# Kernel tuning notes

Hardware: AMD Instinct MI355X
Metric: run time of the kernel (lower is better)

Reference implementation:

```python
import jax, jax.numpy as jnp
import numpy as np

N_NODES = 50000
N_EDGES = 800000
IN_CH, HID_CH, OUT_CH = 512, 128, 64


def gcn_conv(x, W, b, src, dst, num_nodes):
    """PyG GCNConv: add self-loops, sym-normalize, linear, scatter-add, bias.
    x: [N, Fin], W: [Fout, Fin], b: [Fout], src/dst: [E] int."""
    loop = jnp.arange(num_nodes, dtype=src.dtype)
    src2 = jnp.concatenate([src, loop])  # [E+N]
    dst2 = jnp.concatenate([dst, loop])
    deg = jax.ops.segment_sum(jnp.ones_like(dst2, dtype=x.dtype), dst2,
                              num_segments=num_nodes)  # in-degree + 1
    d_inv_sqrt = jnp.where(deg > 0, jax.lax.rsqrt(deg), 0.0)
    norm = d_inv_sqrt[src2] * d_inv_sqrt[dst2]  # [E+N]
    h = x @ W.T  # [N, Fout]
    msg = h[src2] * norm[:, None]  # [E+N, Fout] -- dominant memory traffic
    out = jax.ops.segment_sum(msg, dst2, num_segments=num_nodes)
    return out + b


def setup_inputs() -> dict:
    key = jax.random.key(0)
    ks = jax.random.split(key, 8)
    x = jax.random.normal(ks[0], (N_NODES, IN_CH), dtype=jnp.float32)
    edge_index = jax.random.randint(ks[1], (2, N_EDGES), 0, N_NODES, dtype=jnp.int64)
    s1 = 1.0 / np.sqrt(IN_CH)
    s2 = 1.0 / np.sqrt(HID_CH)
    W1 = jax.random.normal(ks[2], (HID_CH, IN_CH), dtype=jnp.float32) * s1
    b1 = jnp.zeros((HID_CH,), dtype=jnp.float32)
    W_mu = jax.random.normal(ks[3], (OUT_CH, HID_CH), dtype=jnp.float32) * s2
    b_mu = jnp.zeros((OUT_CH,), dtype=jnp.float32)
    W_logstd = jax.random.normal(ks[4], (OUT_CH, HID_CH), dtype=jnp.float32) * s2
    b_logstd = jnp.zeros((OUT_CH,), dtype=jnp.float32)
    return {"x": x, "edge_index": edge_index, "W1": W1, "b1": b1,
            "W_mu": W_mu, "b_mu": b_mu, "W_logstd": W_logstd, "b_logstd": b_logstd}


def reference(x, edge_index, W1, b1, W_mu, b_mu, W_logstd, b_logstd):
    src, dst = edge_index[0], edge_index[1]
    n = x.shape[0]
    h = jax.nn.relu(gcn_conv(x, W1, b1, src, dst, n))
    mu = gcn_conv(h, W_mu, b_mu, src, dst, n)
    logstd = gcn_conv(h, W_logstd, b_logstd, src, dst, n)
    return (mu, logstd)
```

## Files before the change

kernel.cpp:

```cpp
#include <hip/hip_runtime.h>

constexpr int FIN = 512;
constexpr int FH  = 128;
constexpr int FO  = 64;

typedef short short8 __attribute__((ext_vector_type(8)));
typedef float f32x4 __attribute__((ext_vector_type(4)));

__device__ __forceinline__ unsigned short f2bf(float f) {
    unsigned u = __float_as_uint(f);
    u += 0x7fffu + ((u >> 16) & 1u);
    return (unsigned short)(u >> 16);
}
__device__ __forceinline__ float bf2f(unsigned short h) {
    return __uint_as_float((unsigned)h << 16);
}
__device__ __forceinline__ float bflo(unsigned v) { return __uint_as_float(v << 16); }
__device__ __forceinline__ float bfhi(unsigned v) { return __uint_as_float(v & 0xffff0000u); }


__global__ void clear_kernel(int4* __restrict__ p, int n4) {
    int i = blockIdx.x * blockDim.x + threadIdx.x;
    if (i < n4) p[i] = make_int4(0, 0, 0, 0);
}


__global__ void pre_kernel(const int* __restrict__ dst, int* __restrict__ cnt, int E,
                           const float* __restrict__ W1, unsigned short* __restrict__ W1b,
                           const float* __restrict__ Wmu, const float* __restrict__ Wlg,
                           unsigned short* __restrict__ Wh, unsigned short* __restrict__ Wl,
                           int cntB) {
    int b = blockIdx.x;
    if (b < cntB) {
        int i = b * 256 + threadIdx.x;
        if (i < E) atomicAdd(&cnt[dst[i]], 1);
    } else if (b < cntB + 64) {
        int i = (b - cntB) * 256 + threadIdx.x;
        float4 v = ((const float4*)W1)[i];
        ushort4 p;
        p.x = f2bf(v.x); p.y = f2bf(v.y); p.z = f2bf(v.z); p.w = f2bf(v.w);
        ((ushort4*)W1b)[i] = p;
    } else {
        int i = (b - cntB - 64) * 256 + threadIdx.x;
        int r = i >> 7, c = i & 127;
        float f = (r < 64) ? Wmu[r * 128 + c] : Wlg[(r - 64) * 128 + c];
        unsigned short h = f2bf(f);
        Wh[i] = h;
        Wl[i] = f2bf(f - bf2f(h));
    }
}


__global__ void scan1_kernel(const int* __restrict__ cnt, int* __restrict__ offs,
                             int* __restrict__ bsum, float* __restrict__ dinv, int n) {
    __shared__ int sdata[256];
    int t = threadIdx.x;
    int base = blockIdx.x * 1024 + t * 4;
    int4 c = make_int4(0, 0, 0, 0);
    if (base + 3 < n) {
        c = *(const int4*)(cnt + base);
    } else {
        if (base + 0 < n) c.x = cnt[base + 0];
        if (base + 1 < n) c.y = cnt[base + 1];
        if (base + 2 < n) c.z = cnt[base + 2];
        if (base + 3 < n) c.w = cnt[base + 3];
    }
    if (base + 0 < n) dinv[base + 0] = rsqrtf((float)(c.x + 1));
    if (base + 1 < n) dinv[base + 1] = rsqrtf((float)(c.y + 1));
    if (base + 2 < n) dinv[base + 2] = rsqrtf((float)(c.z + 1));
    if (base + 3 < n) dinv[base + 3] = rsqrtf((float)(c.w + 1));

    int s0 = c.x + c.y + c.z + c.w;
    sdata[t] = s0;
    __syncthreads();
    for (int off = 1; off < 256; off <<= 1) {
        int v = (t >= off) ? sdata[t - off] : 0;
        __syncthreads();
        sdata[t] += v;
        __syncthreads();
    }
    int excl = sdata[t] - s0;
    if (t == 255) bsum[blockIdx.x] = sdata[255];
    if (base + 0 < n) offs[base + 0] = excl;
    if (base + 1 < n) offs[base + 1] = excl + c.x;
    if (base + 2 < n) offs[base + 2] = excl + c.x + c.y;
    if (base + 3 < n) offs[base + 3] = excl + c.x + c.y + c.z;
}

__global__ void scan2_kernel(int* __restrict__ bsum, int nb) {
    __shared__ int sdata[256];
    int t = threadIdx.x;
    int v = (t < nb) ? bsum[t] : 0;
    sdata[t] = v;
    __syncthreads();
    for (int off = 1; off < 256; off <<= 1) {
        int u = (t >= off) ? sdata[t - off] : 0;
        __syncthreads();
        sdata[t] += u;
        __syncthreads();
    }
    if (t < nb) bsum[t] = sdata[t] - v;
}

__global__ void scan3_kernel(int* __restrict__ offs, const int* __restrict__ bsum,
                             int n, int E) {
    int i = blockIdx.x * blockDim.x + threadIdx.x;
    if (i < n) offs[i] += bsum[i >> 10];
    if (i == 0) offs[n] = E;
}


__global__ void fill_kernel(const int* __restrict__ src, const int* __restrict__ dst,
                            const float* __restrict__ dinv, const int* __restrict__ offs,
                            int* __restrict__ cnt, int2* __restrict__ esort, int E) {
    int i = blockIdx.x * blockDim.x + threadIdx.x;
    if (i < E) {
        int s = src[i];
        int d = dst[i];
        int old = atomicSub(&cnt[d], 1);
        int pos = offs[d] + old - 1;
        float w = dinv[s] * dinv[d];
        esort[pos] = make_int2(s, __float_as_int(w));
    }
}


__global__ void spmm_kernel(const unsigned int* __restrict__ hin, const int* __restrict__ offs,
                            const int2* __restrict__ esort, const float* __restrict__ dinv,
                            const float* __restrict__ bias, unsigned int* __restrict__ hout,
                            int n, int relu) {
    int gid = blockIdx.x * blockDim.x + threadIdx.x;
    int node = gid >> 6;
    int lane = threadIdx.x & 63;
    if (node >= n) return;
    float di = dinv[node];
    unsigned hv = hin[(size_t)node * 64 + lane];
    float ax = di * di * bflo(hv);
    float ay = di * di * bfhi(hv);
    int p = offs[node];
    int end = offs[node + 1];
    if ((p & 1) && p < end) {
        int2 e = esort[p];
        unsigned v = hin[(size_t)e.x * 64 + lane];
        float w = __int_as_float(e.y);
        ax = fmaf(w, bflo(v), ax); ay = fmaf(w, bfhi(v), ay);
        ++p;
    }
    for (; p + 8 <= end; p += 8) {
        int4 q0 = *(const int4*)(esort + p + 0);
        int4 q1 = *(const int4*)(esort + p + 2);
        int4 q2 = *(const int4*)(esort + p + 4);
        int4 q3 = *(const int4*)(esort + p + 6);
        unsigned v0 = hin[(size_t)q0.x * 64 + lane];
        unsigned v1 = hin[(size_t)q0.z * 64 + lane];
        unsigned v2 = hin[(size_t)q1.x * 64 + lane];
        unsigned v3 = hin[(size_t)q1.z * 64 + lane];
        unsigned v4 = hin[(size_t)q2.x * 64 + lane];
        unsigned v5 = hin[(size_t)q2.z * 64 + lane];
        unsigned v6 = hin[(size_t)q3.x * 64 + lane];
        unsigned v7 = hin[(size_t)q3.z * 64 + lane];
        float w0 = __int_as_float(q0.y), w1 = __int_as_float(q0.w);
        float w2 = __int_as_float(q1.y), w3 = __int_as_float(q1.w);
        float w4 = __int_as_float(q2.y), w5 = __int_as_float(q2.w);
        float w6 = __int_as_float(q3.y), w7 = __int_as_float(q3.w);
        ax = fmaf(w0, bflo(v0), ax); ay = fmaf(w0, bfhi(v0), ay);
        ax = fmaf(w1, bflo(v1), ax); ay = fmaf(w1, bfhi(v1), ay);
        ax = fmaf(w2, bflo(v2), ax); ay = fmaf(w2, bfhi(v2), ay);
        ax = fmaf(w3, bflo(v3), ax); ay = fmaf(w3, bfhi(v3), ay);
        ax = fmaf(w4, bflo(v4), ax); ay = fmaf(w4, bfhi(v4), ay);
        ax = fmaf(w5, bflo(v5), ax); ay = fmaf(w5, bfhi(v5), ay);
        ax = fmaf(w6, bflo(v6), ax); ay = fmaf(w6, bfhi(v6), ay);
        ax = fmaf(w7, bflo(v7), ax); ay = fmaf(w7, bfhi(v7), ay);
    }
    for (; p + 2 <= end; p += 2) {
        int4 q = *(const int4*)(esort + p);
        unsigned v0 = hin[(size_t)q.x * 64 + lane];
        unsigned v1 = hin[(size_t)q.z * 64 + lane];
        float w0 = __int_as_float(q.y), w1 = __int_as_float(q.w);
        ax = fmaf(w0, bflo(v0), ax); ay = fmaf(w0, bfhi(v0), ay);
        ax = fmaf(w1, bflo(v1), ax); ay = fmaf(w1, bfhi(v1), ay);
    }
    if (p < end) {
        int2 e = esort[p];
        unsigned v = hin[(size_t)e.x * 64 + lane];
        float w = __int_as_float(e.y);
        ax = fmaf(w, bflo(v), ax); ay = fmaf(w, bfhi(v), ay);
    }
    if (bias) {
        float2 b = ((const float2*)bias)[lane];
        ax += b.x; ay += b.y;
    }
    if (relu) { ax = fmaxf(ax, 0.f); ay = fmaxf(ay, 0.f); }
    unsigned o = (unsigned)f2bf(ax) | ((unsigned)f2bf(ay) << 16);
    hout[(size_t)node * 64 + lane] = o;
}


__global__ __launch_bounds__(1024, 4) void gemm1_kernel(
    const float* __restrict__ X, const unsigned short* __restrict__ Wb,
    unsigned short* __restrict__ out, int M, int nstrips) {
    extern __shared__ __align__(16) unsigned short Bs[];
    int tid = threadIdx.x;

    #pragma unroll
    for (int j = 0; j < 8; ++j) {
        int f = tid + j * 1024;
        int row = f >> 6;
        unsigned addr = ((unsigned)f << 4) ^ ((unsigned)(row & 7) << 4);
        *(short8*)((char*)Bs + addr) = ((const short8*)Wb)[f];
    }
    __syncthreads();

    int lane = tid & 63, wid = tid >> 6;
    int fr = lane & 15, fq = lane >> 4;
    int s = wid * gridDim.x + blockIdx.x;
    if (s >= nstrips) return;
    int row0 = s * 16;
    int arow = row0 + fr; if (arow >= M) arow = M - 1;
    const float* ap = X + (size_t)arow * FIN + fq * 8;

    f32x4 acc[8] = {};

    float4 c0 = *(const float4*)(ap + 0);
    float4 c1 = *(const float4*)(ap + 4);
    float4 c2 = *(const float4*)(ap + 32);
    float4 c3 = *(const float4*)(ap + 36);

    #pragma unroll
    for (int kk = 0; kk < 8; ++kk) {
        int k0 = kk * 64;
        float4 d0 = c0, d1 = c1, d2 = c2, d3 = c3;
        if (kk < 7) {
            c0 = *(const float4*)(ap + k0 + 64);
            c1 = *(const float4*)(ap + k0 + 68);
            c2 = *(const float4*)(ap + k0 + 96);
            c3 = *(const float4*)(ap + k0 + 100);
        }
        short8 af0, af1;
        af0[0] = (short)f2bf(d0.x); af0[1] = (short)f2bf(d0.y);
        af0[2] = (short)f2bf(d0.z); af0[3] = (short)f2bf(d0.w);
        af0[4] = (short)f2bf(d1.x); af0[5] = (short)f2bf(d1.y);
        af0[6] = (short)f2bf(d1.z); af0[7] = (short)f2bf(d1.w);
        af1[0] = (short)f2bf(d2.x); af1[1] = (short)f2bf(d2.y);
        af1[2] = (short)f2bf(d2.z); af1[3] = (short)f2bf(d2.w);
        af1[4] = (short)f2bf(d3.x); af1[5] = (short)f2bf(d3.y);
        af1[6] = (short)f2bf(d3.z); af1[7] = (short)f2bf(d3.w);

        int cb0 = k0 * 2 + fq * 16;
        #pragma unroll
        for (int c = 0; c < 8; ++c) {
            int br = c * 16 + fr;
            short8 b0 = *(const short8*)((const char*)Bs + br * 1024 +
                                         ((unsigned)cb0 ^ ((unsigned)(br & 7) << 4)));
            acc[c] = __builtin_amdgcn_mfma_f32_16x16x32_bf16(af0, b0, acc[c], 0, 0, 0);
        }
        int cb1 = cb0 + 64;
        #pragma unroll
        for (int c = 0; c < 8; ++c) {
            int br = c * 16 + fr;
            short8 b1 = *(const short8*)((const char*)Bs + br * 1024 +
                                         ((unsigned)cb1 ^ ((unsigned)(br & 7) << 4)));
            acc[c] = __builtin_amdgcn_mfma_f32_16x16x32_bf16(af1, b1, acc[c], 0, 0, 0);
        }
    }

    #pragma unroll
    for (int c = 0; c < 8; ++c) {
        #pragma unroll
        for (int j = 0; j < 4; ++j) {
            int row = row0 + fq * 4 + j;
            if (row < M) out[(size_t)row * FH + c * 16 + fr] = f2bf(acc[c][j]);
        }
    }
}


__global__ __launch_bounds__(512) void gemm2_kernel(
    const unsigned short* __restrict__ Xb,
    const unsigned short* __restrict__ Wh, const unsigned short* __restrict__ Wl,
    float* __restrict__ outA, float* __restrict__ outB,
    const float* __restrict__ biasA, const float* __restrict__ biasB,
    int M, int nstrips) {
    __shared__ __align__(16) unsigned short WhS[128 * 128];
    __shared__ __align__(16) unsigned short WlS[128 * 128];
    int tid = threadIdx.x;

    #pragma unroll
    for (int j = 0; j < 4; ++j) {
        int f = tid + j * 512;
        int row = f >> 4;
        unsigned addr = ((unsigned)f * 16u) ^ ((unsigned)(row & 7) << 4);
        *(short8*)((char*)WhS + addr) = ((const short8*)Wh)[f];
        *(short8*)((char*)WlS + addr) = ((const short8*)Wl)[f];
    }
    __syncthreads();

    int lane = tid & 63, wid = tid >> 6;
    int fr = lane & 15, fq = lane >> 4;
    int s = blockIdx.x * 8 + wid;
    if (s >= nstrips) return;
    int row0 = s * 16;
    int arow = row0 + fr; if (arow > M - 1) arow = M - 1;
    const unsigned short* ap = Xb + (size_t)arow * FH + fq * 8;

    short8 a0 = *(const short8*)(ap + 0);
    short8 a1 = *(const short8*)(ap + 32);
    short8 a2 = *(const short8*)(ap + 64);
    short8 a3 = *(const short8*)(ap + 96);

    f32x4 acc[8] = {};

    auto proc = [&](int k0, short8 a) {
        int cb = k0 * 2 + fq * 16;
        #pragma unroll
        for (int c = 0; c < 8; ++c) {
            int lr = c * 16 + fr;
            unsigned addr = ((unsigned)(lr * 256 + cb)) ^ ((unsigned)(lr & 7) << 4);
            short8 bh = *(const short8*)((const char*)WhS + addr);
            short8 bl = *(const short8*)((const char*)WlS + addr);
            acc[c] = __builtin_amdgcn_mfma_f32_16x16x32_bf16(a, bh, acc[c], 0, 0, 0);
            acc[c] = __builtin_amdgcn_mfma_f32_16x16x32_bf16(a, bl, acc[c], 0, 0, 0);
        }
    };
    proc(0, a0);
    proc(32, a1);
    proc(64, a2);
    proc(96, a3);

    #pragma unroll
    for (int c = 0; c < 8; ++c) {
        float* outp = (c < 4) ? outA : outB;
        const float* bp = (c < 4) ? biasA : biasB;
        int col = (c & 3) * 16 + fr;
        float bv = bp[col];
        #pragma unroll
        for (int j = 0; j < 4; ++j) {
            int row = row0 + fq * 4 + j;
            if (row < M) outp[(size_t)row * FO + col] = acc[c][j] + bv;
        }
    }
}


extern "C" void kernel_launch(void* const* d_in, const int* in_sizes, int n_in,
                              void* d_out, int out_size, void* d_ws, size_t ws_size,
                              hipStream_t stream) {
    const float* x   = (const float*)d_in[0];
    const int*   ei  = (const int*)d_in[1];
    const float* W1  = (const float*)d_in[2];
    const float* b1  = (const float*)d_in[3];
    const float* Wmu = (const float*)d_in[4];
    const float* bmu = (const float*)d_in[5];
    const float* Wlg = (const float*)d_in[6];
    const float* blg = (const float*)d_in[7];

    const int n = in_sizes[0] / FIN;
    const int E = in_sizes[1] / 2;
    const int* src = ei;
    const int* dst = ei + E;
    const int nstrips = (n + 15) / 16;

    char* ws = (char*)d_ws;
    size_t off = 0;
    auto alloc = [&](size_t bytes) -> void* {
        void* p = ws + off;
        off = (off + bytes + 255) & ~((size_t)255);
        return p;
    };
    int*   cnt    = (int*)  alloc((size_t)(n + 4) * 4);
    int*   offs   = (int*)  alloc((size_t)(n + 1) * 4);
    int*   bsum   = (int*)  alloc(1024);
    float* dinv   = (float*)alloc((size_t)n * 4);
    int2*  esort  = (int2*) alloc((size_t)E * 8);
    unsigned short* hbf  = (unsigned short*)alloc((size_t)n * FH * 2);
    unsigned short* h1bf = (unsigned short*)alloc((size_t)n * FH * 2);
    unsigned short* ah2b = (unsigned short*)alloc((size_t)n * FH * 2);
    unsigned short* W1b = (unsigned short*)alloc((size_t)FH * FIN * 2);
    unsigned short* W2h = (unsigned short*)alloc((size_t)FH * FH * 2);
    unsigned short* W2l = (unsigned short*)alloc((size_t)FH * FH * 2);

    int n4 = (n + 3) / 4;
    clear_kernel<<<(n4 + 255) / 256, 256, 0, stream>>>((int4*)cnt, n4);

    int cntB = (E + 255) / 256;
    pre_kernel<<<cntB + 128, 256, 0, stream>>>(dst, cnt, E, W1, W1b, Wmu, Wlg, W2h, W2l, cntB);

    int nb = (n + 1023) / 1024;
    scan1_kernel<<<nb, 256, 0, stream>>>(cnt, offs, bsum, dinv, n);
    scan2_kernel<<<1, 256, 0, stream>>>(bsum, nb);
    scan3_kernel<<<(n + 255) / 256, 256, 0, stream>>>(offs, bsum, n, E);

    fill_kernel<<<(E + 255) / 256, 256, 0, stream>>>(src, dst, dinv, offs, cnt, esort, E);

    gemm1_kernel<<<256, 1024, 128 * 1024, stream>>>(x, W1b, hbf, n, nstrips);
    spmm_kernel<<<(n + 3) / 4, 256, 0, stream>>>(
        (const unsigned*)hbf, offs, esort, dinv, b1, (unsigned*)h1bf, n, 1);
    spmm_kernel<<<(n + 3) / 4, 256, 0, stream>>>(
        (const unsigned*)h1bf, offs, esort, dinv, nullptr, (unsigned*)ah2b, n, 0);
    float* outmu = (float*)d_out;
    float* outlg = outmu + (size_t)n * FO;
    gemm2_kernel<<<(nstrips + 7) / 8, 512, 0, stream>>>(
        ah2b, W2h, W2l, outmu, outlg, bmu, blg, n, nstrips);
}
```

Before: 194.8 us.

## Fuse second-layer aggregation with the mu/logstd GEMM in one kernel

The second sparse aggregation and the final dual-head GEMM are merged into one kernel. Each 1024-thread block aggregates 16 nodes into shared memory, then eight waves run MFMA against the hi/lo bf16 weight copies staged in LDS and write mu and logstd with bias added. This removes the intermediate aggregated buffer's global write and read and one kernel launch. In exchange every block reloads 64KB of weights from L2 and uses 68KB of LDS, which limits occupancy and adds a lot of redundant weight traffic.

```diff
diff --git a/kernel.cpp b/kernel.cpp
--- a/kernel.cpp
+++ b/kernel.cpp
@@ -196,6 +196,119 @@
 }
 
 
+__global__ __launch_bounds__(1024) void spmm2g_kernel(
+    const unsigned int* __restrict__ hin, const int* __restrict__ offs,
+    const int2* __restrict__ esort, const float* __restrict__ dinv,
+    const unsigned short* __restrict__ Wh, const unsigned short* __restrict__ Wl,
+    const float* __restrict__ bmu, const float* __restrict__ blg,
+    float* __restrict__ outmu, float* __restrict__ outlg, int n) {
+    extern __shared__ __align__(16) char smem[];
+    unsigned short* WhS = (unsigned short*)smem;
+    unsigned short* WlS = (unsigned short*)(smem + 32768);
+    unsigned*       rows = (unsigned*)(smem + 65536);
+
+    int tid = threadIdx.x;
+    #pragma unroll
+    for (int j = 0; j < 2; ++j) {
+        int f = tid + j * 1024;
+        int row = f >> 4;
+        unsigned addr = ((unsigned)f * 16u) ^ ((unsigned)(row & 7) << 4);
+        *(short8*)((char*)WhS + addr) = ((const short8*)Wh)[f];
+        *(short8*)((char*)WlS + addr) = ((const short8*)Wl)[f];
+    }
+
+    int wid = tid >> 6, lane = tid & 63;
+    int node = blockIdx.x * 16 + wid;
+
+    float ax = 0.f, ay = 0.f;
+    if (node < n) {
+        float di = dinv[node];
+        unsigned hv = hin[(size_t)node * 64 + lane];
+        ax = di * di * bflo(hv);
+        ay = di * di * bfhi(hv);
+        int p = offs[node];
+        int end = offs[node + 1];
+        if ((p & 1) && p < end) {
+            int2 e = esort[p];
+            unsigned v = hin[(size_t)e.x * 64 + lane];
+            float w = __int_as_float(e.y);
+            ax = fmaf(w, bflo(v), ax); ay = fmaf(w, bfhi(v), ay);
+            ++p;
+        }
+        for (; p + 8 <= end; p += 8) {
+            int4 q0 = *(const int4*)(esort + p + 0);
+            int4 q1 = *(const int4*)(esort + p + 2);
+            int4 q2 = *(const int4*)(esort + p + 4);
+            int4 q3 = *(const int4*)(esort + p + 6);
+            unsigned v0 = hin[(size_t)q0.x * 64 + lane];
+            unsigned v1 = hin[(size_t)q0.z * 64 + lane];
+            unsigned v2 = hin[(size_t)q1.x * 64 + lane];
+            unsigned v3 = hin[(size_t)q1.z * 64 + lane];
+            unsigned v4 = hin[(size_t)q2.x * 64 + lane];
+            unsigned v5 = hin[(size_t)q2.z * 64 + lane];
+            unsigned v6 = hin[(size_t)q3.x * 64 + lane];
+            unsigned v7 = hin[(size_t)q3.z * 64 + lane];
+            float w0 = __int_as_float(q0.y), w1 = __int_as_float(q0.w);
+            float w2 = __int_as_float(q1.y), w3 = __int_as_float(q1.w);
+            float w4 = __int_as_float(q2.y), w5 = __int_as_float(q2.w);
+            float w6 = __int_as_float(q3.y), w7 = __int_as_float(q3.w);
+            ax = fmaf(w0, bflo(v0), ax); ay = fmaf(w0, bfhi(v0), ay);
+            ax = fmaf(w1, bflo(v1), ax); ay = fmaf(w1, bfhi(v1), ay);
+            ax = fmaf(w2, bflo(v2), ax); ay = fmaf(w2, bfhi(v2), ay);
+            ax = fmaf(w3, bflo(v3), ax); ay = fmaf(w3, bfhi(v3), ay);
+            ax = fmaf(w4, bflo(v4), ax); ay = fmaf(w4, bfhi(v4), ay);
+            ax = fmaf(w5, bflo(v5), ax); ay = fmaf(w5, bfhi(v5), ay);
+            ax = fmaf(w6, bflo(v6), ax); ay = fmaf(w6, bfhi(v6), ay);
+            ax = fmaf(w7, bflo(v7), ax); ay = fmaf(w7, bfhi(v7), ay);
+        }
+        for (; p + 2 <= end; p += 2) {
+            int4 q = *(const int4*)(esort + p);
+            unsigned v0 = hin[(size_t)q.x * 64 + lane];
+            unsigned v1 = hin[(size_t)q.z * 64 + lane];
+            float w0 = __int_as_float(q.y), w1 = __int_as_float(q.w);
+            ax = fmaf(w0, bflo(v0), ax); ay = fmaf(w0, bfhi(v0), ay);
+            ax = fmaf(w1, bflo(v1), ax); ay = fmaf(w1, bfhi(v1), ay);
+        }
+        if (p < end) {
+            int2 e = esort[p];
+            unsigned v = hin[(size_t)e.x * 64 + lane];
+            float w = __int_as_float(e.y);
+            ax = fmaf(w, bflo(v), ax); ay = fmaf(w, bfhi(v), ay);
+        }
+    }
+    unsigned o = (unsigned)f2bf(ax) | ((unsigned)f2bf(ay) << 16);
+    rows[wid * 64 + (lane ^ ((wid & 7) << 2))] = o;
+    __syncthreads();
+
+    if (wid < 8) {
+        int fr = lane & 15, fq = lane >> 4;
+        f32x4 acc = {};
+        #pragma unroll
+        for (int ks = 0; ks < 4; ++ks) {
+            int cb = ks * 64 + fq * 16;
+            int r = fr;
+            short8 a = *(const short8*)((const char*)rows + r * 256 +
+                                        ((unsigned)cb ^ ((unsigned)(r & 7) << 4)));
+            int lr = wid * 16 + fr;
+            unsigned baddr = ((unsigned)(lr * 256 + cb)) ^ ((unsigned)(lr & 7) << 4);
+            short8 bh = *(const short8*)((const char*)WhS + baddr);
+            short8 bl = *(const short8*)((const char*)WlS + baddr);
+            acc = __builtin_amdgcn_mfma_f32_16x16x32_bf16(a, bh, acc, 0, 0, 0);
+            acc = __builtin_amdgcn_mfma_f32_16x16x32_bf16(a, bl, acc, 0, 0, 0);
+        }
+        float* outp = (wid < 4) ? outmu : outlg;
+        const float* bp = (wid < 4) ? bmu : blg;
+        int col = (wid & 3) * 16 + fr;
+        float bv = bp[col];
+        #pragma unroll
+        for (int j = 0; j < 4; ++j) {
+            int nrow = blockIdx.x * 16 + fq * 4 + j;
+            if (nrow < n) outp[(size_t)nrow * FO + col] = acc[j] + bv;
+        }
+    }
+}
+
+
 __global__ __launch_bounds__(1024, 4) void gemm1_kernel(
     const float* __restrict__ X, const unsigned short* __restrict__ Wb,
     unsigned short* __restrict__ out, int M, int nstrips) {
@@ -270,73 +383,6 @@
         for (int j = 0; j < 4; ++j) {
             int row = row0 + fq * 4 + j;
             if (row < M) out[(size_t)row * FH + c * 16 + fr] = f2bf(acc[c][j]);
-        }
-    }
-}
-
-
-__global__ __launch_bounds__(512) void gemm2_kernel(
-    const unsigned short* __restrict__ Xb,
-    const unsigned short* __restrict__ Wh, const unsigned short* __restrict__ Wl,
-    float* __restrict__ outA, float* __restrict__ outB,
-    const float* __restrict__ biasA, const float* __restrict__ biasB,
-    int M, int nstrips) {
-    __shared__ __align__(16) unsigned short WhS[128 * 128];
-    __shared__ __align__(16) unsigned short WlS[128 * 128];
-    int tid = threadIdx.x;
-
-    #pragma unroll
-    for (int j = 0; j < 4; ++j) {
-        int f = tid + j * 512;
-        int row = f >> 4;
-        unsigned addr = ((unsigned)f * 16u) ^ ((unsigned)(row & 7) << 4);
-        *(short8*)((char*)WhS + addr) = ((const short8*)Wh)[f];
-        *(short8*)((char*)WlS + addr) = ((const short8*)Wl)[f];
-    }
-    __syncthreads();
-
-    int lane = tid & 63, wid = tid >> 6;
-    int fr = lane & 15, fq = lane >> 4;
-    int s = blockIdx.x * 8 + wid;
-    if (s >= nstrips) return;
-    int row0 = s * 16;
-    int arow = row0 + fr; if (arow > M - 1) arow = M - 1;
-    const unsigned short* ap = Xb + (size_t)arow * FH + fq * 8;
-
-    short8 a0 = *(const short8*)(ap + 0);
-    short8 a1 = *(const short8*)(ap + 32);
-    short8 a2 = *(const short8*)(ap + 64);
-    short8 a3 = *(const short8*)(ap + 96);
-
-    f32x4 acc[8] = {};
-
-    auto proc = [&](int k0, short8 a) {
-        int cb = k0 * 2 + fq * 16;
-        #pragma unroll
-        for (int c = 0; c < 8; ++c) {
-            int lr = c * 16 + fr;
-            unsigned addr = ((unsigned)(lr * 256 + cb)) ^ ((unsigned)(lr & 7) << 4);
-            short8 bh = *(const short8*)((const char*)WhS + addr);
-            short8 bl = *(const short8*)((const char*)WlS + addr);
-            acc[c] = __builtin_amdgcn_mfma_f32_16x16x32_bf16(a, bh, acc[c], 0, 0, 0);
-            acc[c] = __builtin_amdgcn_mfma_f32_16x16x32_bf16(a, bl, acc[c], 0, 0, 0);
-        }
-    };
-    proc(0, a0);
-    proc(32, a1);
-    proc(64, a2);
-    proc(96, a3);
-
-    #pragma unroll
-    for (int c = 0; c < 8; ++c) {
-        float* outp = (c < 4) ? outA : outB;
-        const float* bp = (c < 4) ? biasA : biasB;
-        int col = (c & 3) * 16 + fr;
-        float bv = bp[col];
-        #pragma unroll
-        for (int j = 0; j < 4; ++j) {
-            int row = row0 + fq * 4 + j;
-            if (row < M) outp[(size_t)row * FO + col] = acc[c][j] + bv;
         }
     }
 }
@@ -374,7 +420,6 @@
     int2*  esort  = (int2*) alloc((size_t)E * 8);
     unsigned short* hbf  = (unsigned short*)alloc((size_t)n * FH * 2);
     unsigned short* h1bf = (unsigned short*)alloc((size_t)n * FH * 2);
-    unsigned short* ah2b = (unsigned short*)alloc((size_t)n * FH * 2);
     unsigned short* W1b = (unsigned short*)alloc((size_t)FH * FIN * 2);
     unsigned short* W2h = (unsigned short*)alloc((size_t)FH * FH * 2);
     unsigned short* W2l = (unsigned short*)alloc((size_t)FH * FH * 2);
@@ -395,10 +440,9 @@
     gemm1_kernel<<<256, 1024, 128 * 1024, stream>>>(x, W1b, hbf, n, nstrips);
     spmm_kernel<<<(n + 3) / 4, 256, 0, stream>>>(
         (const unsigned*)hbf, offs, esort, dinv, b1, (unsigned*)h1bf, n, 1);
-    spmm_kernel<<<(n + 3) / 4, 256, 0, stream>>>(
-        (const unsigned*)h1bf, offs, esort, dinv, nullptr, (unsigned*)ah2b, n, 0);
     float* outmu = (float*)d_out;
     float* outlg = outmu + (size_t)n * FO;
-    gemm2_kernel<<<(nstrips + 7) / 8, 512, 0, stream>>>(
-        ah2b, W2h, W2l, outmu, outlg, bmu, blg, n, nstrips);
-}
+    int gblocks = (n + 15) / 16;
+    spmm2g_kernel<<<gblocks, 1024, 68 * 1024, stream>>>(
+        (const unsigned*)h1bf, offs, esort, dinv, W2h, W2l, bmu, blg, outmu, outlg, n);
+}
```

Result: slower. 201.4 us (+3.4%).

## Fuse CSR build and weight conversion into one cooperative kernel with grid syncs

Applied to the files above, without the earlier changes.

Replaces six small kernels (clear, count/convert, three-stage scan, fill) with a single cooperative kernel of 1024 blocks that uses grid.sync between phases. The aim is to remove kernel launch gaps and the tail of each small launch. In exchange, the grid-stride loops run on a fixed grid, and every grid barrier adds a global synchronisation cost.

```diff
diff --git a/kernel.cpp b/kernel.cpp
--- a/kernel.cpp
+++ b/kernel.cpp
@@ -1,4 +1,5 @@
 #include <hip/hip_runtime.h>
+#include <hip/hip_cooperative_groups.h>
 
 constexpr int FIN = 512;
 constexpr int FH  = 128;
@@ -19,102 +20,95 @@
 __device__ __forceinline__ float bfhi(unsigned v) { return __uint_as_float(v & 0xffff0000u); }
 
 
-__global__ void clear_kernel(int4* __restrict__ p, int n4) {
-    int i = blockIdx.x * blockDim.x + threadIdx.x;
-    if (i < n4) p[i] = make_int4(0, 0, 0, 0);
-}
-
-
-__global__ void pre_kernel(const int* __restrict__ dst, int* __restrict__ cnt, int E,
-                           const float* __restrict__ W1, unsigned short* __restrict__ W1b,
-                           const float* __restrict__ Wmu, const float* __restrict__ Wlg,
-                           unsigned short* __restrict__ Wh, unsigned short* __restrict__ Wl,
-                           int cntB) {
-    int b = blockIdx.x;
-    if (b < cntB) {
-        int i = b * 256 + threadIdx.x;
-        if (i < E) atomicAdd(&cnt[dst[i]], 1);
-    } else if (b < cntB + 64) {
-        int i = (b - cntB) * 256 + threadIdx.x;
+__global__ void build_kernel(const int* __restrict__ src, const int* __restrict__ dst,
+                             int E, int n,
+                             const float* __restrict__ W1, unsigned short* __restrict__ W1b,
+                             const float* __restrict__ Wmu, const float* __restrict__ Wlg,
+                             unsigned short* __restrict__ W2h, unsigned short* __restrict__ W2l,
+                             int* __restrict__ cnt, int* __restrict__ offs,
+                             int* __restrict__ bsum, float* __restrict__ dinv,
+                             int2* __restrict__ esort) {
+    namespace cg = cooperative_groups;
+    cg::grid_group grid = cg::this_grid();
+    __shared__ int sdata[256];
+
+    int tid = threadIdx.x;
+    int gtid = blockIdx.x * blockDim.x + tid;
+    int gthreads = gridDim.x * blockDim.x;
+
+    for (int i = gtid; i < n; i += gthreads) cnt[i] = 0;
+    for (int i = gtid; i < FH * FIN / 4; i += gthreads) {
         float4 v = ((const float4*)W1)[i];
         ushort4 p;
         p.x = f2bf(v.x); p.y = f2bf(v.y); p.z = f2bf(v.z); p.w = f2bf(v.w);
         ((ushort4*)W1b)[i] = p;
-    } else {
-        int i = (b - cntB - 64) * 256 + threadIdx.x;
+    }
+    for (int i = gtid; i < FH * FH; i += gthreads) {
         int r = i >> 7, c = i & 127;
         float f = (r < 64) ? Wmu[r * 128 + c] : Wlg[(r - 64) * 128 + c];
         unsigned short h = f2bf(f);
-        Wh[i] = h;
-        Wl[i] = f2bf(f - bf2f(h));
-    }
-}
-
-
-__global__ void scan1_kernel(const int* __restrict__ cnt, int* __restrict__ offs,
-                             int* __restrict__ bsum, float* __restrict__ dinv, int n) {
-    __shared__ int sdata[256];
-    int t = threadIdx.x;
-    int base = blockIdx.x * 1024 + t * 4;
-    int4 c = make_int4(0, 0, 0, 0);
-    if (base + 3 < n) {
-        c = *(const int4*)(cnt + base);
-    } else {
-        if (base + 0 < n) c.x = cnt[base + 0];
-        if (base + 1 < n) c.y = cnt[base + 1];
-        if (base + 2 < n) c.z = cnt[base + 2];
-        if (base + 3 < n) c.w = cnt[base + 3];
-    }
-    if (base + 0 < n) dinv[base + 0] = rsqrtf((float)(c.x + 1));
-    if (base + 1 < n) dinv[base + 1] = rsqrtf((float)(c.y + 1));
-    if (base + 2 < n) dinv[base + 2] = rsqrtf((float)(c.z + 1));
-    if (base + 3 < n) dinv[base + 3] = rsqrtf((float)(c.w + 1));
-
-    int s0 = c.x + c.y + c.z + c.w;
-    sdata[t] = s0;
-    __syncthreads();
-    for (int off = 1; off < 256; off <<= 1) {
-        int v = (t >= off) ? sdata[t - off] : 0;
+        W2h[i] = h;
+        W2l[i] = f2bf(f - bf2f(h));
+    }
+    grid.sync();
+
+    for (int i = gtid; i < E; i += gthreads) atomicAdd(&cnt[dst[i]], 1);
+    grid.sync();
+
+    int nb = (n + 1023) >> 10;
+    if (blockIdx.x < nb) {
+        int base = blockIdx.x * 1024 + tid * 4;
+        int4 c = make_int4(0, 0, 0, 0);
+        if (base + 3 < n) {
+            c = *(const int4*)(cnt + base);
+        } else {
+            if (base + 0 < n) c.x = cnt[base + 0];
+            if (base + 1 < n) c.y = cnt[base + 1];
+            if (base + 2 < n) c.z = cnt[base + 2];
+            if (base + 3 < n) c.w = cnt[base + 3];
+        }
+        if (base + 0 < n) dinv[base + 0] = rsqrtf((float)(c.x + 1));
+        if (base + 1 < n) dinv[base + 1] = rsqrtf((float)(c.y + 1));
+        if (base + 2 < n) dinv[base + 2] = rsqrtf((float)(c.z + 1));
+        if (base + 3 < n) dinv[base + 3] = rsqrtf((float)(c.w + 1));
+
+        int s0 = c.x + c.y + c.z + c.w;
+        sdata[tid] = s0;
         __syncthreads();
-        sdata[t] += v;
+        for (int off = 1; off < 256; off <<= 1) {
+            int v = (tid >= off) ? sdata[tid - off] : 0;
+            __syncthreads();
+            sdata[tid] += v;
+            __syncthreads();
+        }
+        int excl = sdata[tid] - s0;
+        if (tid == 255) bsum[blockIdx.x] = sdata[255];
+        if (base + 0 < n) offs[base + 0] = excl;
+        if (base + 1 < n) offs[base + 1] = excl + c.x;
+        if (base + 2 < n) offs[base + 2] = excl + c.x + c.y;
+        if (base + 3 < n) offs[base + 3] = excl + c.x + c.y + c.z;
+    }
+    grid.sync();
+
+    if (blockIdx.x == 0) {
+        int v = (tid < nb) ? bsum[tid] : 0;
+        sdata[tid] = v;
         __syncthreads();
-    }
-    int excl = sdata[t] - s0;
-    if (t == 255) bsum[blockIdx.x] = sdata[255];
-    if (base + 0 < n) offs[base + 0] = excl;
-    if (base + 1 < n) offs[base + 1] = excl + c.x;
-    if (base + 2 < n) offs[base + 2] = excl + c.x + c.y;
-    if (base + 3 < n) offs[base + 3] = excl + c.x + c.y + c.z;
-}
-
-__global__ void scan2_kernel(int* __restrict__ bsum, int nb) {
-    __shared__ int sdata[256];
-    int t = threadIdx.x;
-    int v = (t < nb) ? bsum[t] : 0;
-    sdata[t] = v;
-    __syncthreads();
-    for (int off = 1; off < 256; off <<= 1) {
-        int u = (t >= off) ? sdata[t - off] : 0;
-        __syncthreads();
-        sdata[t] += u;
-        __syncthreads();
-    }
-    if (t < nb) bsum[t] = sdata[t] - v;
-}
-
-__global__ void scan3_kernel(int* __restrict__ offs, const int* __restrict__ bsum,
-                             int n, int E) {
-    int i = blockIdx.x * blockDim.x + threadIdx.x;
-    if (i < n) offs[i] += bsum[i >> 10];
-    if (i == 0) offs[n] = E;
-}
-
-
-__global__ void fill_kernel(const int* __restrict__ src, const int* __restrict__ dst,
-                            const float* __restrict__ dinv, const int* __restrict__ offs,
-                            int* __restrict__ cnt, int2* __restrict__ esort, int E) {
-    int i = blockIdx.x * blockDim.x + threadIdx.x;
-    if (i < E) {
+        for (int off = 1; off < 256; off <<= 1) {
+            int u = (tid >= off) ? sdata[tid - off] : 0;
+            __syncthreads();
+            sdata[tid] += u;
+            __syncthreads();
+        }
+        if (tid < nb) bsum[tid] = sdata[tid] - v;
+    }
+    grid.sync();
+
+    for (int i = gtid; i < n; i += gthreads) offs[i] += bsum[i >> 10];
+    if (gtid == 0) offs[n] = E;
+    grid.sync();
+
+    for (int i = gtid; i < E; i += gthreads) {
         int s = src[i];
         int d = dst[i];
         int old = atomicSub(&cnt[d], 1);
@@ -354,8 +348,8 @@
     const float* Wlg = (const float*)d_in[6];
     const float* blg = (const float*)d_in[7];
 
-    const int n = in_sizes[0] / FIN;
-    const int E = in_sizes[1] / 2;
+    int n = in_sizes[0] / FIN;
+    int E = in_sizes[1] / 2;
     const int* src = ei;
     const int* dst = ei + E;
     const int nstrips = (n + 15) / 16;
@@ -379,18 +373,13 @@
     unsigned short* W2h = (unsigned short*)alloc((size_t)FH * FH * 2);
     unsigned short* W2l = (unsigned short*)alloc((size_t)FH * FH * 2);
 
-    int n4 = (n + 3) / 4;
-    clear_kernel<<<(n4 + 255) / 256, 256, 0, stream>>>((int4*)cnt, n4);
-
-    int cntB = (E + 255) / 256;
-    pre_kernel<<<cntB + 128, 256, 0, stream>>>(dst, cnt, E, W1, W1b, Wmu, Wlg, W2h, W2l, cntB);
-
-    int nb = (n + 1023) / 1024;
-    scan1_kernel<<<nb, 256, 0, stream>>>(cnt, offs, bsum, dinv, n);
-    scan2_kernel<<<1, 256, 0, stream>>>(bsum, nb);
-    scan3_kernel<<<(n + 255) / 256, 256, 0, stream>>>(offs, bsum, n, E);
-
-    fill_kernel<<<(E + 255) / 256, 256, 0, stream>>>(src, dst, dinv, offs, cnt, esort, E);
+    void* args[] = {(void*)&src, (void*)&dst, (void*)&E, (void*)&n,
+                    (void*)&W1, (void*)&W1b, (void*)&Wmu, (void*)&Wlg,
+                    (void*)&W2h, (void*)&W2l,
+                    (void*)&cnt, (void*)&offs, (void*)&bsum, (void*)&dinv,
+                    (void*)&esort};
+    hipLaunchCooperativeKernel((void*)build_kernel, dim3(1024), dim3(256),
+                               args, 0, stream);
 
     gemm1_kernel<<<256, 1024, 128 * 1024, stream>>>(x, W1b, hbf, n, nstrips);
     spmm_kernel<<<(n + 3) / 4, 256, 0, stream>>>(
```

Result: slower. 666.8 us (+242.2%).
